# Kernel tuning notes

Measured on AMD Instinct MI355X. Metric: run time of the kernel, lower is better.

Reference implementation:

```python
import jax, jax.numpy as jnp
import numpy as np

N = 6144
ATTR = 512
HID = 256
EMB = 16
ALPHA = 0.2  # LeakyReLU negative slope
NEG_INF = -9e15


def setup_inputs() -> dict:
    key = jax.random.key(0)
    ks = jax.random.split(key, 9)
    x = jax.random.normal(ks[0], (N, ATTR), dtype=jnp.float32)
    # sparse-ish binary adjacency (avg degree ~30), stored dense as the module expects
    adj = (jax.random.uniform(ks[1], (N, N)) < 0.005).astype(jnp.float32)
    M = jax.random.uniform(ks[2], (N, N), dtype=jnp.float32)
    W1 = jax.random.normal(ks[3], (ATTR, HID), dtype=jnp.float32) * 0.05
    a_self1 = jax.random.normal(ks[4], (HID, 1), dtype=jnp.float32) * 0.05
    a_neigh1 = jax.random.normal(ks[5], (HID, 1), dtype=jnp.float32) * 0.05
    W2 = jax.random.normal(ks[6], (HID, EMB), dtype=jnp.float32) * 0.05
    a_self2 = jax.random.normal(ks[7], (EMB, 1), dtype=jnp.float32) * 0.05
    a_neigh2 = jax.random.normal(ks[8], (EMB, 1), dtype=jnp.float32) * 0.05
    return {"x": x, "adj": adj, "M": M, "W1": W1, "a_self1": a_self1,
            "a_neigh1": a_neigh1, "W2": W2, "a_self2": a_self2, "a_neigh2": a_neigh2}


def gate_layer(h_in, adj, M, W, a_self, a_neigh):
    h = h_in @ W                                   # [N, F]
    f_self = h @ a_self                            # [N, 1]
    f_neigh = h @ a_neigh                          # [N, 1]
    e = jax.nn.leaky_relu((f_self + f_neigh.T) * M, negative_slope=ALPHA)  # [N, N]
    e = jnp.where(adj > 0, e, NEG_INF)
    attn = jax.nn.softmax(e, axis=1)
    return jax.nn.elu(attn @ h)


def reference(x, adj, M, W1, a_self1, a_neigh1, W2, a_self2, a_neigh2):
    h = gate_layer(x, adj, M, W1, a_self1, a_neigh1)
    h = gate_layer(h, adj, M, W2, a_self2, a_neigh2)
    # F.normalize(h, p=2, dim=1)
    norm = jnp.maximum(jnp.linalg.norm(h, axis=1, keepdims=True), 1e-12)
    z = h / norm                                    # [N, EMB]
    s = z @ z.T                                     # [N, N]
    A_pred = jax.nn.sigmoid(s - 1.0 / s)
    return A_pred, z
```

## Files before the change

### kernel.cpp

```cpp
#include <hip/hip_runtime.h>
#include <math.h>

#define N 6144
#define ATTR 512
#define HID 256
#define EMB 16
#define ALPHA 0.2f
#define MAXDEG 192
#define BK 16
#define GEMM_BLOCKS ((N / 64) * (HID / 64))

typedef float f32x4v __attribute__((ext_vector_type(4)));

__global__ __launch_bounds__(256) void k_fused(const float* __restrict__ x,
                                               const float* __restrict__ W1,
                                               float* __restrict__ h1,
                                               const float* __restrict__ adj,
                                               const float* __restrict__ Mm,
                                               int* __restrict__ nbr,
                                               float* __restrict__ mval,
                                               int* __restrict__ deg) {
  __shared__ float AsT[2][BK][68];
  __shared__ float Bs[2][BK][68];
  __shared__ int wcnt[N / 1024][4];
  __shared__ int nbidx[MAXDEG];
  const int tid = threadIdx.x;

  if (blockIdx.x < GEMM_BLOCKS) {
    const int b = blockIdx.x;
    const int ct = b & 3;
    const int rt = b >> 2;
    const int tx = tid & 15;
    const int ty = tid >> 4;
    const int row0 = rt * 64, col0 = ct * 64;
    const int ar = tid >> 2;
    const int akq = (tid & 3) * 4;
    const int bk = tid >> 4;
    const int bc = (tid & 15) * 4;
    float4 pa = *(const float4*)&x[(size_t)(row0 + ar) * ATTR + akq];
    float4 pb = *(const float4*)&W1[(size_t)bk * HID + col0 + bc];
    float acc[4][4] = {};
    int buf = 0;
    for (int kt = 0; kt < ATTR; kt += BK) {
      AsT[buf][akq + 0][ar] = pa.x;
      AsT[buf][akq + 1][ar] = pa.y;
      AsT[buf][akq + 2][ar] = pa.z;
      AsT[buf][akq + 3][ar] = pa.w;
      *(float4*)&Bs[buf][bk][bc] = pb;
      __syncthreads();
      if (kt + BK < ATTR) {
        pa = *(const float4*)&x[(size_t)(row0 + ar) * ATTR + kt + BK + akq];
        pb = *(const float4*)&W1[(size_t)(kt + BK + bk) * HID + col0 + bc];
      }
#pragma unroll
      for (int k = 0; k < BK; ++k) {
        const float4 a = *(const float4*)&AsT[buf][k][ty * 4];
        const float4 b4 = *(const float4*)&Bs[buf][k][tx * 4];
        acc[0][0] += a.x * b4.x; acc[0][1] += a.x * b4.y; acc[0][2] += a.x * b4.z; acc[0][3] += a.x * b4.w;
        acc[1][0] += a.y * b4.x; acc[1][1] += a.y * b4.y; acc[1][2] += a.y * b4.z; acc[1][3] += a.y * b4.w;
        acc[2][0] += a.z * b4.x; acc[2][1] += a.z * b4.y; acc[2][2] += a.z * b4.z; acc[2][3] += a.z * b4.w;
        acc[3][0] += a.w * b4.x; acc[3][1] += a.w * b4.y; acc[3][2] += a.w * b4.z; acc[3][3] += a.w * b4.w;
      }
      buf ^= 1;
    }
#pragma unroll
    for (int i = 0; i < 4; ++i) {
      float4 o = {acc[i][0], acc[i][1], acc[i][2], acc[i][3]};
      *(float4*)&h1[(size_t)(row0 + ty * 4 + i) * HID + col0 + tx * 4] = o;
    }
    return;
  }

  const int i = blockIdx.x - GEMM_BLOCKS;
  const int w = tid >> 6, lane = tid & 63;
  const float4* arow = (const float4*)(adj + (size_t)i * N);
  int* nrow = nbr + (size_t)i * MAXDEG;
  float4 av[N / 1024];
#pragma unroll
  for (int r = 0; r < N / 1024; ++r) av[r] = arow[r * 256 + tid];
  unsigned long long m1[N / 1024], m2[N / 1024], m3[N / 1024], m4[N / 1024];
#pragma unroll
  for (int r = 0; r < N / 1024; ++r) {
    const float4 a = av[r];
    bool h0 = a.x > 0.f, h1b = a.y > 0.f, h2b = a.z > 0.f, h3b = a.w > 0.f;
    int cnt = (int)h0 + (int)h1b + (int)h2b + (int)h3b;
    m1[r] = __ballot(cnt >= 1);
    m2[r] = __ballot(cnt >= 2);
    m3[r] = __ballot(cnt >= 3);
    m4[r] = __ballot(cnt >= 4);
    if (lane == 0) {
      wcnt[r][w] = __popcll(m1[r]) + __popcll(m2[r]) + __popcll(m3[r]) + __popcll(m4[r]);
    }
  }
  __syncthreads();
  const unsigned long long lt = (1ull << lane) - 1ull;
  int count = 0;
#pragma unroll
  for (int r = 0; r < N / 1024; ++r) {
    const float4 a = av[r];
    bool h0 = a.x > 0.f, h1b = a.y > 0.f, h2b = a.z > 0.f, h3b = a.w > 0.f;
    int woff = 0;
#pragma unroll
    for (int q = 0; q < 4; ++q) woff += (q < w) ? wcnt[r][q] : 0;
    int pos = count + woff + __popcll(m1[r] & lt) + __popcll(m2[r] & lt) +
              __popcll(m3[r] & lt) + __popcll(m4[r] & lt);
    const int idx = r * 1024 + tid * 4;
    if (h0) { if (pos < MAXDEG) { nrow[pos] = idx;     nbidx[pos] = idx;     } ++pos; }
    if (h1b){ if (pos < MAXDEG) { nrow[pos] = idx + 1; nbidx[pos] = idx + 1; } ++pos; }
    if (h2b){ if (pos < MAXDEG) { nrow[pos] = idx + 2; nbidx[pos] = idx + 2; } ++pos; }
    if (h3b){ if (pos < MAXDEG) { nrow[pos] = idx + 3; nbidx[pos] = idx + 3; } ++pos; }
    count += wcnt[r][0] + wcnt[r][1] + wcnt[r][2] + wcnt[r][3];
  }
  if (tid == 0) deg[i] = count > MAXDEG ? MAXDEG : count;
  __syncthreads();
  const int d = count > MAXDEG ? MAXDEG : count;
  const float* mrow = Mm + (size_t)i * N;
  float* mout = mval + (size_t)i * MAXDEG;
  for (int s = tid; s < d; s += 256) mout[s] = mrow[nbidx[s]];
}

__global__ __launch_bounds__(256) void k_f1(const float* __restrict__ h1,
                                            const float* __restrict__ a_s,
                                            const float* __restrict__ a_n,
                                            float* __restrict__ f1s,
                                            float* __restrict__ f1n) {
  const int wid = (blockIdx.x * 256 + threadIdx.x) >> 6;
  const int lane = threadIdx.x & 63;
  const float* hrow = h1 + (size_t)wid * HID;
  float ss = 0.0f, sn = 0.0f;
#pragma unroll
  for (int c0 = 0; c0 < HID; c0 += 64) {
    float h = hrow[c0 + lane];
    ss += h * a_s[c0 + lane];
    sn += h * a_n[c0 + lane];
  }
#pragma unroll
  for (int off = 32; off; off >>= 1) {
    ss += __shfl_xor(ss, off);
    sn += __shfl_xor(sn, off);
  }
  if (lane == 0) { f1s[wid] = ss; f1n[wid] = sn; }
}

__global__ __launch_bounds__(256) void k_attn1(const float* __restrict__ h1,
                                               const float* __restrict__ f1s,
                                               const float* __restrict__ f1n,
                                               const int* __restrict__ nbr,
                                               const float* __restrict__ mval,
                                               const int* __restrict__ deg,
                                               float* __restrict__ out1) {
  __shared__ float p[MAXDEG];
  __shared__ int nb[MAXDEG];
  const int i = blockIdx.x;
  const int tid = threadIdx.x;
  const int d = deg[i];
  if (d > 0 && tid < 64) {
    const float fsi = f1s[i];
    float lmax = -3.0e38f;
    for (int j = tid; j < d; j += 64) {
      int nj = nbr[(size_t)i * MAXDEG + j];
      nb[j] = nj;
      float v = (fsi + f1n[nj]) * mval[(size_t)i * MAXDEG + j];
      float e = v > 0.0f ? v : ALPHA * v;
      p[j] = e;
      lmax = fmaxf(lmax, e);
    }
#pragma unroll
    for (int off = 32; off; off >>= 1) lmax = fmaxf(lmax, __shfl_xor(lmax, off));
    float lsum = 0.0f;
    for (int j = tid; j < d; j += 64) {
      float t = expf(p[j] - lmax);
      p[j] = t;
      lsum += t;
    }
#pragma unroll
    for (int off = 32; off; off >>= 1) lsum += __shfl_xor(lsum, off);
    float inv = 1.0f / lsum;
    for (int j = tid; j < d; j += 64) p[j] *= inv;
  }
  __syncthreads();
  float acc = 0.0f;
  if (d > 0) {
    for (int j = 0; j < d; ++j) {
      acc += p[j] * h1[(size_t)nb[j] * HID + tid];
    }
  } else {
    for (int j = 0; j < N; ++j) acc += h1[(size_t)j * HID + tid];
    acc *= (1.0f / (float)N);
  }
  out1[(size_t)i * HID + tid] = acc > 0.0f ? acc : expm1f(acc);
}

__global__ __launch_bounds__(256) void k_gemm2(const float* __restrict__ out1,
                                               const float* __restrict__ W2,
                                               const float* __restrict__ a_s,
                                               const float* __restrict__ a_n,
                                               float* __restrict__ h2,
                                               float* __restrict__ f2s,
                                               float* __restrict__ f2n) {
  __shared__ float Hs[16][HID + 1];
  __shared__ float Ws[HID][EMB + 1];
  const int row0 = blockIdx.x * 16;
  const int tid = threadIdx.x;
  for (int l = tid; l < 16 * HID; l += 256) {
    Hs[l >> 8][l & 255] = out1[(size_t)(row0 + (l >> 8)) * HID + (l & 255)];
  }
  for (int l = tid; l < HID * EMB; l += 256) {
    Ws[l >> 4][l & 15] = W2[l];
  }
  __syncthreads();
  const int r = tid >> 4, c = tid & 15;
  float acc = 0.0f;
  for (int k = 0; k < HID; ++k) acc += Hs[r][k] * Ws[k][c];
  h2[(size_t)(row0 + r) * EMB + c] = acc;
  float vs = acc * a_s[c], vn = acc * a_n[c];
#pragma unroll
  for (int off = 1; off < 16; off <<= 1) {
    vs += __shfl_xor(vs, off);
    vn += __shfl_xor(vn, off);
  }
  if (c == 0) { f2s[row0 + r] = vs; f2n[row0 + r] = vn; }
}

__global__ __launch_bounds__(256) void k_attn2(const float* __restrict__ h2,
                                               const float* __restrict__ f2s,
                                               const float* __restrict__ f2n,
                                               const int* __restrict__ nbr,
                                               const float* __restrict__ mval,
                                               const int* __restrict__ deg,
                                               float* __restrict__ z) {
  __shared__ float p[4][MAXDEG];
  __shared__ int nb[4][MAXDEG];
  const int w = threadIdx.x >> 6, lane = threadIdx.x & 63;
  const int i = blockIdx.x * 4 + w;
  const int d = deg[i];
  if (d > 0) {
    const float fsi = f2s[i];
    float lmax = -3.0e38f;
    for (int j = lane; j < d; j += 64) {
      int nj = nbr[(size_t)i * MAXDEG + j];
      nb[w][j] = nj;
      float v = (fsi + f2n[nj]) * mval[(size_t)i * MAXDEG + j];
      float e = v > 0.0f ? v : ALPHA * v;
      p[w][j] = e;
      lmax = fmaxf(lmax, e);
    }
#pragma unroll
    for (int off = 32; off; off >>= 1) lmax = fmaxf(lmax, __shfl_xor(lmax, off));
    float lsum = 0.0f;
    for (int j = lane; j < d; j += 64) {
      float t = expf(p[w][j] - lmax);
      p[w][j] = t;
      lsum += t;
    }
#pragma unroll
    for (int off = 32; off; off >>= 1) lsum += __shfl_xor(lsum, off);
    float inv = 1.0f / lsum;
    for (int j = lane; j < d; j += 64) p[w][j] *= inv;
  }
  __syncthreads();
  const int g = lane >> 4, c = lane & 15;
  float acc = 0.0f;
  if (d > 0) {
    for (int j = g; j < d; j += 4) {
      acc += p[w][j] * h2[(size_t)nb[w][j] * EMB + c];
    }
  } else {
    for (int j = g; j < N; j += 4) acc += h2[(size_t)j * EMB + c];
  }
  acc += __shfl_xor(acc, 16);
  acc += __shfl_xor(acc, 32);
  if (d == 0) acc *= (1.0f / (float)N);
  float val = acc > 0.0f ? acc : expm1f(acc);
  float sq = val * val;
#pragma unroll
  for (int off = 1; off < 16; off <<= 1) sq += __shfl_xor(sq, off);
  float nrm = fmaxf(sqrtf(sq), 1e-12f);
  float zv = val / nrm;
  if (lane < 16) z[(size_t)i * EMB + lane] = zv;
}

__device__ __forceinline__ float sig_of(float s) {
  float t = s - 1.0f / s;
  return 1.0f / (1.0f + expf(-t));
}

__global__ __launch_bounds__(256) void k_apred(const float* __restrict__ z,
                                               float* __restrict__ A) {
  __shared__ float zi_s[8 * EMB];
  const int i0 = blockIdx.y * 8;
  const int tid = threadIdx.x;
  if (tid < 8 * EMB) zi_s[tid] = z[(size_t)i0 * EMB + tid];
  const int j0 = blockIdx.x * 1024 + tid * 4;
  float zj[4][EMB];
  const float4* zp = (const float4*)(z + (size_t)j0 * EMB);
#pragma unroll
  for (int q = 0; q < 4; ++q) {
#pragma unroll
    for (int kk = 0; kk < 4; ++kk) {
      float4 v = zp[q * 4 + kk];
      zj[q][kk * 4 + 0] = v.x;
      zj[q][kk * 4 + 1] = v.y;
      zj[q][kk * 4 + 2] = v.z;
      zj[q][kk * 4 + 3] = v.w;
    }
  }
  __syncthreads();
  for (int ii = 0; ii < 8; ++ii) {
    float acc0 = 0.0f, acc1 = 0.0f, acc2 = 0.0f, acc3 = 0.0f;
#pragma unroll
    for (int k = 0; k < EMB; ++k) {
      float a = zi_s[ii * EMB + k];
      acc0 += a * zj[0][k];
      acc1 += a * zj[1][k];
      acc2 += a * zj[2][k];
      acc3 += a * zj[3][k];
    }
    f32x4v o;
    o.x = sig_of(acc0);
    o.y = sig_of(acc1);
    o.z = sig_of(acc2);
    o.w = sig_of(acc3);
    __builtin_nontemporal_store(o, (f32x4v*)(A + (size_t)(i0 + ii) * N + j0));
  }
}

extern "C" void kernel_launch(void* const* d_in, const int* in_sizes, int n_in,
                              void* d_out, int out_size, void* d_ws, size_t ws_size,
                              hipStream_t stream) {
  const float* x   = (const float*)d_in[0];
  const float* adj = (const float*)d_in[1];
  const float* Mm  = (const float*)d_in[2];
  const float* W1  = (const float*)d_in[3];
  const float* a1s = (const float*)d_in[4];
  const float* a1n = (const float*)d_in[5];
  const float* W2  = (const float*)d_in[6];
  const float* a2s = (const float*)d_in[7];
  const float* a2n = (const float*)d_in[8];

  float* out = (float*)d_out;
  float* h1   = out;
  float* out1 = h1 + (size_t)N * HID;
  float* h2   = out1 + (size_t)N * HID;
  float* f1s  = h2 + (size_t)N * EMB;
  float* f1n  = f1s + N;
  float* f2s  = f1n + N;
  float* f2n  = f2s + N;
  float* mval = f2n + N;
  int*   nbr  = (int*)(mval + (size_t)N * MAXDEG);
  int*   deg  = nbr + (size_t)N * MAXDEG;
  float* z    = out + (size_t)N * N;
  float* A    = out;

  hipLaunchKernelGGL(k_fused, dim3(GEMM_BLOCKS + N), dim3(256), 0, stream,
                     x, W1, h1, adj, Mm, nbr, mval, deg);
  hipLaunchKernelGGL(k_f1, dim3(N / 4), dim3(256), 0, stream, h1, a1s, a1n, f1s, f1n);
  hipLaunchKernelGGL(k_attn1, dim3(N), dim3(256), 0, stream, h1, f1s, f1n, nbr, mval, deg, out1);
  hipLaunchKernelGGL(k_gemm2, dim3(N / 16), dim3(256), 0, stream, out1, W2, a2s, a2n, h2, f2s, f2n);
  hipLaunchKernelGGL(k_attn2, dim3(N / 4), dim3(256), 0, stream, h2, f2s, f2n, nbr, mval, deg, z);
  hipLaunchKernelGGL(k_apred, dim3(N / 1024, N / 8), dim3(256), 0, stream, z, A);
}
```

Before: 140.4 us.

## Widen layer-1 GEMM tile to 64x128 and stream adjacency with nontemporal loads

The fused kernel's GEMM blocks now compute 64x128 output tiles, with 8 columns per thread instead of 4. This halves the number of GEMM blocks and improves reuse of the A tile. The adjacency-scan path loads rows and gathers M with nontemporal loads to avoid polluting cache. It also recomputes ballots in the second pass instead of keeping mask arrays in registers, which cuts register pressure. The wider accumulator raises GEMM register use and LDS size.

Measured after the change: 152.3 us. 1.09x slower.

```diff
diff --git a/kernel.cpp b/kernel.cpp
--- a/kernel.cpp
+++ b/kernel.cpp
@@ -8,7 +8,7 @@
 #define ALPHA 0.2f
 #define MAXDEG 192
 #define BK 16
-#define GEMM_BLOCKS ((N / 64) * (HID / 64))
+#define GEMM_BLOCKS ((N / 64) * (HID / 128))
 
 typedef float f32x4v __attribute__((ext_vector_type(4)));
 
@@ -21,75 +21,86 @@
                                                float* __restrict__ mval,
                                                int* __restrict__ deg) {
   __shared__ float AsT[2][BK][68];
-  __shared__ float Bs[2][BK][68];
+  __shared__ float Bs[2][BK][132];
   __shared__ int wcnt[N / 1024][4];
   __shared__ int nbidx[MAXDEG];
   const int tid = threadIdx.x;
 
   if (blockIdx.x < GEMM_BLOCKS) {
     const int b = blockIdx.x;
-    const int ct = b & 3;
-    const int rt = b >> 2;
+    const int ct = b & 1;
+    const int rt = b >> 1;
     const int tx = tid & 15;
     const int ty = tid >> 4;
-    const int row0 = rt * 64, col0 = ct * 64;
+    const int row0 = rt * 64, col0 = ct * 128;
     const int ar = tid >> 2;
     const int akq = (tid & 3) * 4;
     const int bk = tid >> 4;
     const int bc = (tid & 15) * 4;
     float4 pa = *(const float4*)&x[(size_t)(row0 + ar) * ATTR + akq];
-    float4 pb = *(const float4*)&W1[(size_t)bk * HID + col0 + bc];
-    float acc[4][4] = {};
+    float4 pb0 = *(const float4*)&W1[(size_t)bk * HID + col0 + bc];
+    float4 pb1 = *(const float4*)&W1[(size_t)bk * HID + col0 + 64 + bc];
+    float acc[4][8] = {};
     int buf = 0;
     for (int kt = 0; kt < ATTR; kt += BK) {
       AsT[buf][akq + 0][ar] = pa.x;
       AsT[buf][akq + 1][ar] = pa.y;
       AsT[buf][akq + 2][ar] = pa.z;
       AsT[buf][akq + 3][ar] = pa.w;
-      *(float4*)&Bs[buf][bk][bc] = pb;
+      *(float4*)&Bs[buf][bk][bc] = pb0;
+      *(float4*)&Bs[buf][bk][64 + bc] = pb1;
       __syncthreads();
       if (kt + BK < ATTR) {
         pa = *(const float4*)&x[(size_t)(row0 + ar) * ATTR + kt + BK + akq];
-        pb = *(const float4*)&W1[(size_t)(kt + BK + bk) * HID + col0 + bc];
+        pb0 = *(const float4*)&W1[(size_t)(kt + BK + bk) * HID + col0 + bc];
+        pb1 = *(const float4*)&W1[(size_t)(kt + BK + bk) * HID + col0 + 64 + bc];
       }
 #pragma unroll
       for (int k = 0; k < BK; ++k) {
         const float4 a = *(const float4*)&AsT[buf][k][ty * 4];
-        const float4 b4 = *(const float4*)&Bs[buf][k][tx * 4];
-        acc[0][0] += a.x * b4.x; acc[0][1] += a.x * b4.y; acc[0][2] += a.x * b4.z; acc[0][3] += a.x * b4.w;
-        acc[1][0] += a.y * b4.x; acc[1][1] += a.y * b4.y; acc[1][2] += a.y * b4.z; acc[1][3] += a.y * b4.w;
-        acc[2][0] += a.z * b4.x; acc[2][1] += a.z * b4.y; acc[2][2] += a.z * b4.z; acc[2][3] += a.z * b4.w;
-        acc[3][0] += a.w * b4.x; acc[3][1] += a.w * b4.y; acc[3][2] += a.w * b4.z; acc[3][3] += a.w * b4.w;
+        const float4 b0 = *(const float4*)&Bs[buf][k][tx * 4];
+        const float4 b1 = *(const float4*)&Bs[buf][k][64 + tx * 4];
+        acc[0][0] += a.x * b0.x; acc[0][1] += a.x * b0.y; acc[0][2] += a.x * b0.z; acc[0][3] += a.x * b0.w;
+        acc[1][0] += a.y * b0.x; acc[1][1] += a.y * b0.y; acc[1][2] += a.y * b0.z; acc[1][3] += a.y * b0.w;
+        acc[2][0] += a.z * b0.x; acc[2][1] += a.z * b0.y; acc[2][2] += a.z * b0.z; acc[2][3] += a.z * b0.w;
+        acc[3][0] += a.w * b0.x; acc[3][1] += a.w * b0.y; acc[3][2] += a.w * b0.z; acc[3][3] += a.w * b0.w;
+        acc[0][4] += a.x * b1.x; acc[0][5] += a.x * b1.y; acc[0][6] += a.x * b1.z; acc[0][7] += a.x * b1.w;
+        acc[1][4] += a.y * b1.x; acc[1][5] += a.y * b1.y; acc[1][6] += a.y * b1.z; acc[1][7] += a.y * b1.w;
+        acc[2][4] += a.z * b1.x; acc[2][5] += a.z * b1.y; acc[2][6] += a.z * b1.z; acc[2][7] += a.z * b1.w;
+        acc[3][4] += a.w * b1.x; acc[3][5] += a.w * b1.y; acc[3][6] += a.w * b1.z; acc[3][7] += a.w * b1.w;
       }
       buf ^= 1;
     }
 #pragma unroll
     for (int i = 0; i < 4; ++i) {
-      float4 o = {acc[i][0], acc[i][1], acc[i][2], acc[i][3]};
-      *(float4*)&h1[(size_t)(row0 + ty * 4 + i) * HID + col0 + tx * 4] = o;
+      float4 o0 = {acc[i][0], acc[i][1], acc[i][2], acc[i][3]};
+      float4 o1 = {acc[i][4], acc[i][5], acc[i][6], acc[i][7]};
+      *(float4*)&h1[(size_t)(row0 + ty * 4 + i) * HID + col0 + tx * 4] = o0;
+      *(float4*)&h1[(size_t)(row0 + ty * 4 + i) * HID + col0 + 64 + tx * 4] = o1;
     }
     return;
   }
 
   const int i = blockIdx.x - GEMM_BLOCKS;
   const int w = tid >> 6, lane = tid & 63;
-  const float4* arow = (const float4*)(adj + (size_t)i * N);
+  const f32x4v* arow = (const f32x4v*)(adj + (size_t)i * N);
   int* nrow = nbr + (size_t)i * MAXDEG;
-  float4 av[N / 1024];
-#pragma unroll
-  for (int r = 0; r < N / 1024; ++r) av[r] = arow[r * 256 + tid];
-  unsigned long long m1[N / 1024], m2[N / 1024], m3[N / 1024], m4[N / 1024];
+  f32x4v av[N / 1024];
 #pragma unroll
   for (int r = 0; r < N / 1024; ++r) {
-    const float4 a = av[r];
+    av[r] = __builtin_nontemporal_load(arow + r * 256 + tid);
+  }
+#pragma unroll
+  for (int r = 0; r < N / 1024; ++r) {
+    const f32x4v a = av[r];
     bool h0 = a.x > 0.f, h1b = a.y > 0.f, h2b = a.z > 0.f, h3b = a.w > 0.f;
     int cnt = (int)h0 + (int)h1b + (int)h2b + (int)h3b;
-    m1[r] = __ballot(cnt >= 1);
-    m2[r] = __ballot(cnt >= 2);
-    m3[r] = __ballot(cnt >= 3);
-    m4[r] = __ballot(cnt >= 4);
+    unsigned long long m1 = __ballot(cnt >= 1);
+    unsigned long long m2 = __ballot(cnt >= 2);
+    unsigned long long m3 = __ballot(cnt >= 3);
+    unsigned long long m4 = __ballot(cnt >= 4);
     if (lane == 0) {
-      wcnt[r][w] = __popcll(m1[r]) + __popcll(m2[r]) + __popcll(m3[r]) + __popcll(m4[r]);
+      wcnt[r][w] = __popcll(m1) + __popcll(m2) + __popcll(m3) + __popcll(m4);
     }
   }
   __syncthreads();
@@ -97,13 +108,18 @@
   int count = 0;
 #pragma unroll
   for (int r = 0; r < N / 1024; ++r) {
-    const float4 a = av[r];
+    const f32x4v a = av[r];
     bool h0 = a.x > 0.f, h1b = a.y > 0.f, h2b = a.z > 0.f, h3b = a.w > 0.f;
+    int cnt = (int)h0 + (int)h1b + (int)h2b + (int)h3b;
+    unsigned long long m1 = __ballot(cnt >= 1);
+    unsigned long long m2 = __ballot(cnt >= 2);
+    unsigned long long m3 = __ballot(cnt >= 3);
+    unsigned long long m4 = __ballot(cnt >= 4);
     int woff = 0;
 #pragma unroll
     for (int q = 0; q < 4; ++q) woff += (q < w) ? wcnt[r][q] : 0;
-    int pos = count + woff + __popcll(m1[r] & lt) + __popcll(m2[r] & lt) +
-              __popcll(m3[r] & lt) + __popcll(m4[r] & lt);
+    int pos = count + woff + __popcll(m1 & lt) + __popcll(m2 & lt) +
+              __popcll(m3 & lt) + __popcll(m4 & lt);
     const int idx = r * 1024 + tid * 4;
     if (h0) { if (pos < MAXDEG) { nrow[pos] = idx;     nbidx[pos] = idx;     } ++pos; }
     if (h1b){ if (pos < MAXDEG) { nrow[pos] = idx + 1; nbidx[pos] = idx + 1; } ++pos; }
@@ -116,7 +132,9 @@
   const int d = count > MAXDEG ? MAXDEG : count;
   const float* mrow = Mm + (size_t)i * N;
   float* mout = mval + (size_t)i * MAXDEG;
-  for (int s = tid; s < d; s += 256) mout[s] = mrow[nbidx[s]];
+  for (int s = tid; s < d; s += 256) {
+    mout[s] = __builtin_nontemporal_load(mrow + nbidx[s]);
+  }
 }
 
 __global__ __launch_bounds__(256) void k_f1(const float* __restrict__ h1,
```
